# Kernel optimization log

Measured on AMD Instinct MI355X. Metric: run time of the kernel, lower is better.

Reference implementation:

```python
import jax, jax.numpy as jnp
import numpy as np

B, T, D, U = 64, 2048, 256, 256

def setup_inputs() -> dict:
    key = jax.random.key(0)
    ks = jax.random.split(key, 8)
    return {
        "query": jax.random.normal(ks[0], (B, D), dtype=jnp.float32),
        "values": jax.random.normal(ks[1], (B, T, D), dtype=jnp.float32),
        "W1_w": jax.random.normal(ks[2], (D, U), dtype=jnp.float32) * 0.05,
        "W1_b": jnp.zeros((U,), dtype=jnp.float32),
        "W2_w": jax.random.normal(ks[3], (D, U), dtype=jnp.float32) * 0.05,
        "W2_b": jnp.zeros((U,), dtype=jnp.float32),
        "V_w": jax.random.normal(ks[4], (U, 1), dtype=jnp.float32) * 0.05,
        "V_b": jnp.zeros((1,), dtype=jnp.float32),
    }

def reference(query, values, W1_w, W1_b, W2_w, W2_b, V_w, V_b):
    # query: [B, D] -> [B, 1, U]
    q_proj = (query @ W1_w + W1_b)[:, None, :]
    # values: [B, T, D] -> [B, T, U]
    v_proj = jnp.einsum('btd,du->btu', values, W2_w) + W2_b
    # score: [B, T, 1]
    score = jnp.tanh(q_proj + v_proj) @ V_w + V_b
    attention_weights = jax.nn.softmax(score, axis=1)  # over time axis
    context_vector = jnp.sum(attention_weights * values, axis=1)  # [B, D]
    return (context_vector, attention_weights)
```

## Files before the change

### kernel.cpp

```cpp
#include <hip/hip_runtime.h>
#include <hip/hip_fp16.h>

#define B_ 64
#define T_ 2048
#define D_ 256
#define U_ 256
#define BT 256
#define NT (BT / 16)
#define TC (T_ / BT)

typedef _Float16 half8  __attribute__((ext_vector_type(8)));
typedef float    floatx4 __attribute__((ext_vector_type(4)));

typedef const __attribute__((address_space(1))) void cg_void;
typedef __attribute__((address_space(3))) void       ls_void;

#define WC_VM8_ONLY   0x0F78
#define WC_LGKM0_ONLY 0xC07F
#define WC_ALL0       0x0070

__global__ void prep_kernel(const float* __restrict__ query,
                            const float* __restrict__ W1_w,
                            const float* __restrict__ W1_b,
                            const float* __restrict__ W2_w,
                            const float* __restrict__ W2_b,
                            float* __restrict__ qb,
                            _Float16* __restrict__ w2t) {
    __shared__ float sh[32 * 33];
    if (blockIdx.x < 64) {
        const int b = blockIdx.x;
        const int u = threadIdx.x;
        sh[u] = query[b * D_ + u];
        __syncthreads();
        float acc = W1_b[u] + W2_b[u];
#pragma unroll 8
        for (int d = 0; d < D_; ++d)
            acc += sh[d] * W1_w[d * U_ + u];
        qb[b * U_ + u] = acc;
    } else {
        const int bid = blockIdx.x - 64;
        const int tu = bid & 7;
        const int td = bid >> 3;
        const int c  = threadIdx.x & 31;
        const int r0 = threadIdx.x >> 5;
        float* tile = sh;
#pragma unroll
        for (int i = 0; i < 4; ++i) {
            int r = r0 + i * 8;
            tile[r * 33 + c] = W2_w[(td * 32 + r) * U_ + tu * 32 + c];
        }
        __syncthreads();
#pragma unroll
        for (int i = 0; i < 4; ++i) {
            int r = r0 + i * 8;
            w2t[(tu * 32 + r) * D_ + td * 32 + c] = (_Float16)tile[c * 33 + r];
        }
    }
}

__launch_bounds__(256, 2)
__global__ void score_ctx_kernel(const float* __restrict__ values,
                                 const _Float16* __restrict__ w2t,
                                 const float* __restrict__ qb,
                                 const float* __restrict__ V_w,
                                 float* __restrict__ wexp,
                                 float* __restrict__ pctx,
                                 float* __restrict__ pl) {
    __shared__ __align__(16) float vbuf[4][16 * D_];
    __shared__ float s_part[2][16][4];

    const int b     = blockIdx.y;
    const int chunk = blockIdx.x;
    const int tid   = threadIdx.x;
    const int wave  = tid >> 6;
    const int lane  = tid & 63;
    const int n16   = lane & 15;
    const int quad  = lane >> 4;
    const int u0    = wave * 64;

    half8 bfrag[4][8];
#pragma unroll
    for (int ut = 0; ut < 4; ++ut) {
        const int u = u0 + ut * 16 + n16;
#pragma unroll
        for (int k = 0; k < 8; ++k)
            bfrag[ut][k] = *(const half8*)(w2t + u * D_ + k * 32 + quad * 8);
    }
    float qbv[4], vwv[4];
#pragma unroll
    for (int ut = 0; ut < 4; ++ut) {
        const int u = u0 + ut * 16 + n16;
        qbv[ut] = qb[b * U_ + u];
        vwv[ut] = V_w[u];
    }

    const float* vbase = values + (size_t)b * T_ * D_ + (size_t)chunk * BT * D_;

    auto stage = [&](int tile, int bi) {
        const float* src = vbase + tile * 16 * D_;
#pragma unroll
        for (int i = 0; i < 4; ++i) {
            const int r = i * 4 + wave;
            const float* g = src + r * D_ + ((lane ^ (r & 7)) << 2);
            float* l = &vbuf[bi][r * D_];
            __builtin_amdgcn_global_load_lds((cg_void*)g, (ls_void*)l, 16, 0, 0);
        }
    };

    stage(0, 0); stage(1, 1); stage(2, 2);

    float c     = 0.f;
    float l_run = 0.f;

    float* wout = wexp + b * T_ + chunk * BT;

    for (int t = 0; t < NT; ++t) {
        __builtin_amdgcn_s_waitcnt(WC_VM8_ONLY);
        __builtin_amdgcn_s_barrier();
        stage((t + 3 < NT) ? t + 3 : t, (t + 3) & 3);

        floatx4 acc[4] = {};
        const float* rowbase = &vbuf[t & 3][n16 * D_];
        const int swz = n16 & 7;
#pragma unroll
        for (int k = 0; k < 8; ++k) {
            const int c0 = k * 8 + quad * 2;
            floatx4 q0 = *(const floatx4*)(rowbase + (((c0    ) ^ swz) << 2));
            floatx4 q1 = *(const floatx4*)(rowbase + (((c0 + 1) ^ swz) << 2));
            half8 a;
            a[0] = (_Float16)q0.x; a[1] = (_Float16)q0.y;
            a[2] = (_Float16)q0.z; a[3] = (_Float16)q0.w;
            a[4] = (_Float16)q1.x; a[5] = (_Float16)q1.y;
            a[6] = (_Float16)q1.z; a[7] = (_Float16)q1.w;
#pragma unroll
            for (int ut = 0; ut < 4; ++ut)
                acc[ut] = __builtin_amdgcn_mfma_f32_16x16x32_f16(a, bfrag[ut][k], acc[ut], 0, 0, 0);
        }

        float part[4];
#pragma unroll
        for (int r = 0; r < 4; ++r) {
            float s = 0.f;
#pragma unroll
            for (int ut = 0; ut < 4; ++ut) {
                float x  = acc[ut][r] + qbv[ut];
                float e  = __expf(2.f * x);
                float th = 1.f - __fdividef(2.f, e + 1.f);
                s += th * vwv[ut];
            }
            part[r] = s;
        }
#pragma unroll
        for (int m = 1; m < 16; m <<= 1)
#pragma unroll
            for (int r = 0; r < 4; ++r)
                part[r] += __shfl_xor(part[r], m, 16);
        if (n16 == 0)
#pragma unroll
            for (int r = 0; r < 4; ++r)
                s_part[t & 1][quad * 4 + r][wave] = part[r];

        __builtin_amdgcn_s_waitcnt(WC_LGKM0_ONLY);
        __builtin_amdgcn_s_barrier();

        const int ccx = tid >> 2, lo = tid & 3;
#pragma unroll
        for (int r = 0; r < 16; ++r) {
            floatx4 sp = *(const floatx4*)&s_part[t & 1][r][0];
            float s = (sp.x + sp.y) + (sp.z + sp.w);
            float w = __expf(s);
            l_run += w;
            c += w * vbuf[t & 3][r * D_ + ((ccx ^ (r & 7)) << 2) + lo];
            if (tid == r) wout[t * 16 + r] = w;
        }
    }

    pctx[(b * TC + chunk) * D_ + tid] = c;
    if (tid == 0) pl[b * TC + chunk] = l_run;
    __builtin_amdgcn_s_waitcnt(WC_ALL0);
}

__global__ void finalize_kernel(const float* __restrict__ pctx,
                                const float* __restrict__ pl,
                                const float* __restrict__ wexp,
                                float* __restrict__ ctx,
                                float* __restrict__ attn) {
    const int b = blockIdx.x, tid = threadIdx.x;
    float L = 0.f;
#pragma unroll
    for (int i = 0; i < TC; ++i) L += pl[b * TC + i];
    const float invL = 1.f / L;
    float s = 0.f;
#pragma unroll
    for (int i = 0; i < TC; ++i) s += pctx[(b * TC + i) * D_ + tid];
    ctx[b * D_ + tid] = s * invL;
#pragma unroll
    for (int j = 0; j < T_ / 256; ++j) {
        const int t = j * 256 + tid;
        attn[b * T_ + t] = wexp[b * T_ + t] * invL;
    }
}

extern "C" void kernel_launch(void* const* d_in, const int* in_sizes, int n_in,
                              void* d_out, int out_size, void* d_ws, size_t ws_size,
                              hipStream_t stream) {
    const float* query  = (const float*)d_in[0];
    const float* values = (const float*)d_in[1];
    const float* W1_w   = (const float*)d_in[2];
    const float* W1_b   = (const float*)d_in[3];
    const float* W2_w   = (const float*)d_in[4];
    const float* W2_b   = (const float*)d_in[5];
    const float* V_w    = (const float*)d_in[6];

    float* out  = (float*)d_out;
    float* ctx  = out;
    float* attn = out + B_ * D_;

    char* ws = (char*)d_ws;
    float*    qb   = (float*)ws;
    _Float16* w2t  = (_Float16*)(ws + (64 << 10));
    float*    wexp = (float*)(ws + (192 << 10));
    float*    pctx = (float*)(ws + (704 << 10));
    float*    pl   = (float*)(ws + (1216 << 10));

    prep_kernel     <<<dim3(128),     dim3(256), 0, stream>>>(query, W1_w, W1_b, W2_w, W2_b, qb, w2t);
    score_ctx_kernel<<<dim3(TC, B_),  dim3(256), 0, stream>>>(values, w2t, qb, V_w, wexp, pctx, pl);
    finalize_kernel <<<dim3(B_),      dim3(256), 0, stream>>>(pctx, pl, wexp, ctx, attn);
}
```

Baseline: 249.9 us.

## Split score/context block across 512 threads with double-buffered LDS staging

The score/context kernel now runs 512 threads per block. Each wave owns 32 of the U columns instead of 64, and the two halves of the block each accumulate the context for 8 of the 16 rows, combining through LDS at the end. The 4-deep async LDS prefetch ring with hand-coded waitcnts is replaced by a 2-buffer scheme using __syncthreads, which shrinks LDS and register use so more waves fit per CU. The cost is less prefetch depth, full-drain barriers each tile, and an extra reduction step.

```diff
diff --git a/kernel.cpp b/kernel.cpp
--- a/kernel.cpp
+++ b/kernel.cpp
@@ -14,10 +14,6 @@
 
 typedef const __attribute__((address_space(1))) void cg_void;
 typedef __attribute__((address_space(3))) void       ls_void;
-
-#define WC_VM8_ONLY   0x0F78
-#define WC_LGKM0_ONLY 0xC07F
-#define WC_ALL0       0x0070
 
 __global__ void prep_kernel(const float* __restrict__ query,
                             const float* __restrict__ W1_w,
@@ -58,7 +54,7 @@
     }
 }
 
-__launch_bounds__(256, 2)
+__launch_bounds__(512, 4)
 __global__ void score_ctx_kernel(const float* __restrict__ values,
                                  const _Float16* __restrict__ w2t,
                                  const float* __restrict__ qb,
@@ -66,8 +62,10 @@
                                  float* __restrict__ wexp,
                                  float* __restrict__ pctx,
                                  float* __restrict__ pl) {
-    __shared__ __align__(16) float vbuf[4][16 * D_];
-    __shared__ float s_part[2][16][4];
+    __shared__ __align__(16) float vbuf[2][16 * D_];
+    __shared__ __align__(16) float s_part[2][16][8];
+    __shared__ float csum[512];
+    __shared__ float lsum[2];
 
     const int b     = blockIdx.y;
     const int chunk = blockIdx.x;
@@ -76,19 +74,19 @@
     const int lane  = tid & 63;
     const int n16   = lane & 15;
     const int quad  = lane >> 4;
-    const int u0    = wave * 64;
-
-    half8 bfrag[4][8];
-#pragma unroll
-    for (int ut = 0; ut < 4; ++ut) {
+    const int u0    = wave * 32;
+
+    half8 bfrag[2][8];
+#pragma unroll
+    for (int ut = 0; ut < 2; ++ut) {
         const int u = u0 + ut * 16 + n16;
 #pragma unroll
         for (int k = 0; k < 8; ++k)
             bfrag[ut][k] = *(const half8*)(w2t + u * D_ + k * 32 + quad * 8);
     }
-    float qbv[4], vwv[4];
-#pragma unroll
-    for (int ut = 0; ut < 4; ++ut) {
+    float qbv[2], vwv[2];
+#pragma unroll
+    for (int ut = 0; ut < 2; ++ut) {
         const int u = u0 + ut * 16 + n16;
         qbv[ut] = qb[b * U_ + u];
         vwv[ut] = V_w[u];
@@ -99,28 +97,30 @@
     auto stage = [&](int tile, int bi) {
         const float* src = vbase + tile * 16 * D_;
 #pragma unroll
-        for (int i = 0; i < 4; ++i) {
-            const int r = i * 4 + wave;
+        for (int i = 0; i < 2; ++i) {
+            const int r = wave * 2 + i;
             const float* g = src + r * D_ + ((lane ^ (r & 7)) << 2);
             float* l = &vbuf[bi][r * D_];
             __builtin_amdgcn_global_load_lds((cg_void*)g, (ls_void*)l, 16, 0, 0);
         }
     };
 
-    stage(0, 0); stage(1, 1); stage(2, 2);
+    stage(0, 0);
 
     float c     = 0.f;
     float l_run = 0.f;
+    const int half = tid >> 8;
+    const int dd   = tid & 255;
+    const int ccx  = dd >> 2, lo = dd & 3;
 
     float* wout = wexp + b * T_ + chunk * BT;
 
     for (int t = 0; t < NT; ++t) {
-        __builtin_amdgcn_s_waitcnt(WC_VM8_ONLY);
-        __builtin_amdgcn_s_barrier();
-        stage((t + 3 < NT) ? t + 3 : t, (t + 3) & 3);
-
-        floatx4 acc[4] = {};
-        const float* rowbase = &vbuf[t & 3][n16 * D_];
+        __syncthreads();
+        if (t + 1 < NT) stage(t + 1, (t + 1) & 1);
+
+        floatx4 acc[2] = {};
+        const float* rowbase = &vbuf[t & 1][n16 * D_];
         const int swz = n16 & 7;
 #pragma unroll
         for (int k = 0; k < 8; ++k) {
@@ -133,7 +133,7 @@
             a[4] = (_Float16)q1.x; a[5] = (_Float16)q1.y;
             a[6] = (_Float16)q1.z; a[7] = (_Float16)q1.w;
 #pragma unroll
-            for (int ut = 0; ut < 4; ++ut)
+            for (int ut = 0; ut < 2; ++ut)
                 acc[ut] = __builtin_amdgcn_mfma_f32_16x16x32_f16(a, bfrag[ut][k], acc[ut], 0, 0, 0);
         }
 
@@ -142,7 +142,7 @@
         for (int r = 0; r < 4; ++r) {
             float s = 0.f;
 #pragma unroll
-            for (int ut = 0; ut < 4; ++ut) {
+            for (int ut = 0; ut < 2; ++ut) {
                 float x  = acc[ut][r] + qbv[ut];
                 float e  = __expf(2.f * x);
                 float th = 1.f - __fdividef(2.f, e + 1.f);
@@ -160,24 +160,27 @@
             for (int r = 0; r < 4; ++r)
                 s_part[t & 1][quad * 4 + r][wave] = part[r];
 
-        __builtin_amdgcn_s_waitcnt(WC_LGKM0_ONLY);
-        __builtin_amdgcn_s_barrier();
-
-        const int ccx = tid >> 2, lo = tid & 3;
-#pragma unroll
-        for (int r = 0; r < 16; ++r) {
-            floatx4 sp = *(const floatx4*)&s_part[t & 1][r][0];
-            float s = (sp.x + sp.y) + (sp.z + sp.w);
+        __syncthreads();
+
+#pragma unroll
+        for (int j = 0; j < 8; ++j) {
+            const int r = half * 8 + j;
+            floatx4 p0 = *(const floatx4*)&s_part[t & 1][r][0];
+            floatx4 p1 = *(const floatx4*)&s_part[t & 1][r][4];
+            float s = ((p0.x + p0.y) + (p0.z + p0.w)) + ((p1.x + p1.y) + (p1.z + p1.w));
             float w = __expf(s);
             l_run += w;
-            c += w * vbuf[t & 3][r * D_ + ((ccx ^ (r & 7)) << 2) + lo];
-            if (tid == r) wout[t * 16 + r] = w;
-        }
-    }
-
-    pctx[(b * TC + chunk) * D_ + tid] = c;
-    if (tid == 0) pl[b * TC + chunk] = l_run;
-    __builtin_amdgcn_s_waitcnt(WC_ALL0);
+            c += w * vbuf[t & 1][r * D_ + ((ccx ^ (r & 7)) << 2) + lo];
+            if (dd == j) wout[t * 16 + r] = w;
+        }
+    }
+
+    __syncthreads();
+    csum[tid] = c;
+    if (dd == 0) lsum[half] = l_run;
+    __syncthreads();
+    if (tid < 256) pctx[(b * TC + chunk) * D_ + tid] = csum[tid] + csum[tid + 256];
+    if (tid == 0)  pl[b * TC + chunk] = lsum[0] + lsum[1];
 }
 
 __global__ void finalize_kernel(const float* __restrict__ pctx,
@@ -224,6 +227,6 @@
     float*    pl   = (float*)(ws + (1216 << 10));
 
     prep_kernel     <<<dim3(128),     dim3(256), 0, stream>>>(query, W1_w, W1_b, W2_w, W2_b, qb, w2t);
-    score_ctx_kernel<<<dim3(TC, B_),  dim3(256), 0, stream>>>(values, w2t, qb, V_w, wexp, pctx, pl);
+    score_ctx_kernel<<<dim3(TC, B_),  dim3(512), 0, stream>>>(values, w2t, qb, V_w, wexp, pctx, pl);
     finalize_kernel <<<dim3(B_),      dim3(256), 0, stream>>>(pctx, pl, wexp, ctx, attn);
 }
```

Result: slower. 288.5 us (+15.4%).
